# Kernel optimization log

Hardware: AMD Instinct MI355X
Metric: run time of the kernel (lower is better)

## Reference

```python
import jax, jax.numpy as jnp
import numpy as np

N_HEAD = 8
D_HEAD = 16
D_MODEL = 128
LEN_Q = 256
MEM_LEN = 256
BATCH = 4


def setup_inputs() -> dict:
    key = jax.random.key(0)
    k1, k2, k3, k4, k5 = jax.random.split(key, 5)
    h = jax.random.normal(k1, (LEN_Q, BATCH, D_MODEL), dtype=jnp.float32)
    mems = jax.random.normal(k2, (MEM_LEN, BATCH, D_MODEL), dtype=jnp.float32)
    # nn.Linear weights are [out_features, in_features]
    Wq = jax.random.normal(k3, (N_HEAD * D_HEAD, D_MODEL), dtype=jnp.float32) / np.sqrt(D_MODEL)
    Wk = jax.random.normal(k4, (N_HEAD * D_HEAD, D_MODEL), dtype=jnp.float32) / np.sqrt(D_MODEL)
    paramR = jax.random.normal(k5, (N_HEAD,), dtype=jnp.float32)
    return {"h": h, "mems": mems, "Wq": Wq, "Wk": Wk, "paramR": paramR}


def reference(h, mems, Wq, Wk, paramR):
    # h: [Lq, B, Dm], mems: [M, B, Dm]
    c = jnp.concatenate([mems, h], axis=0)  # [Lk, B, Dm]
    Lq, B = h.shape[0], h.shape[1]
    Lk = c.shape[0]
    # Linear (no bias): x @ W.T, then split heads and move to [H, B, L, Dh]
    head_q = (h @ Wq.T).reshape(Lq, B, N_HEAD, D_HEAD).transpose(2, 1, 0, 3)
    head_k = (c @ Wk.T).reshape(Lk, B, N_HEAD, D_HEAD).transpose(2, 1, 0, 3)
    # Pairwise difference: [H, B, Lq, Lk, Dh]
    diff = head_q[:, :, :, None, :] - head_k[:, :, None, :, :]
    scaled = diff * paramR[:, None, None, None, None] / jnp.pi
    # torch.sinc == jnp.sinc (normalized sinc, sinc(0)=1)
    score = jnp.abs(jnp.prod(jnp.sinc(scaled), axis=4))  # [H, B, Lq, Lk]
    # permute(2, 3, 1, 0) -> [Lq, Lk, B, H]
    return score.transpose(2, 3, 1, 0)
```

## Files before the change

### kernel.cpp

```cpp
#include <hip/hip_runtime.h>
#include <math.h>

#define LQ 256
#define MEML 256
#define LK 512
#define BB 4
#define NH 8
#define DM 128

#define IT 8
#define QSTRIDE 20

constexpr float INV2PI = 0.15915494309189535f;

__global__ __launch_bounds__(128) void proj_kernel(
    const float* __restrict__ hh, const float* __restrict__ mems,
    const float* __restrict__ Wq, const float* __restrict__ Wk,
    const float* __restrict__ paramR,
    float* __restrict__ qs, float* __restrict__ ksT)
{
    __shared__ float x[8 * 128];
    const int blk = blockIdx.x;
    const int t = threadIdx.x;
    const bool isQ = (blk < 128);
    const int row0 = isQ ? blk * 8 : (blk - 128) * 8;
    const float* __restrict__ W = isQ ? Wq : Wk;

    for (int r = 0; r < 8; ++r) {
        const int row = row0 + r;
        const float* src = isQ ? (hh + row * DM)
                               : ((row < MEML * BB) ? (mems + row * DM)
                                                    : (hh + (row - MEML * BB) * DM));
        x[r * 128 + t] = src[t];
    }
    __syncthreads();

    float acc[8] = {0, 0, 0, 0, 0, 0, 0, 0};
    const float* wrow = W + t * DM;
    for (int k = 0; k < DM; k += 4) {
        const float4 w = *(const float4*)(wrow + k);
        #pragma unroll
        for (int r = 0; r < 8; ++r) {
            acc[r] += x[r * 128 + k + 0] * w.x + x[r * 128 + k + 1] * w.y
                    + x[r * 128 + k + 2] * w.z + x[r * 128 + k + 3] * w.w;
        }
    }
    const int h = t >> 4, d = t & 15;
    const float rs = paramR[h] * INV2PI;
    if (isQ) {
        float* dst = qs + row0 * 128 + t;
        #pragma unroll
        for (int r = 0; r < 8; ++r) dst[r * 128] = acc[r] * rs;
    } else {
        #pragma unroll
        for (int r = 0; r < 8; ++r) {
            const int row = row0 + r;
            const int j = row >> 2, b = row & 3;
            ksT[((d >> 2) * LK + j) * 128 + (b * 8 + h) * 4 + (d & 3)] = acc[r] * rs;
        }
    }
}

__global__ __launch_bounds__(256, 6) void score_kernel(
    const float* __restrict__ qs, const float* __restrict__ ksT,
    float* __restrict__ out)
{
    __shared__ float qt[IT * 32 * QSTRIDE];
    const int t = threadIdx.x;
    const int bh = t & 31;
    const int js = t >> 5;
    const int key = bh >> 3;
    const int i0 = blockIdx.x * IT;
    const int j = blockIdx.y * 8 + js;

    constexpr float i2 = INV2PI * INV2PI;
    constexpr float i4 = i2 * i2;
    constexpr float i8 = i4 * i4;
    constexpr float C16 = i8 * i8;
    constexpr float EPS = 2.0e-4f * INV2PI;

    {
        const float* src = qs + i0 * 32 * 16;
        #pragma unroll
        for (int rep = 0; rep < 4; ++rep) {
            const int c4 = rep * 256 + t;
            const int row = c4 >> 2, cc = (c4 & 3) * 4;
            const float4 v = *(const float4*)(src + c4 * 4);
            *(float4*)(&qt[row * QSTRIDE + cc]) = v;
        }
    }

    float k[16];
    #pragma unroll
    for (int s = 0; s < 4; ++s) {
        const int plane = s ^ key;
        const float4 v = *(const float4*)(ksT + (plane * LK + j) * 128 + bh * 4);
        k[s * 4 + 0] = v.x; k[s * 4 + 1] = v.y;
        k[s * 4 + 2] = v.z; k[s * 4 + 3] = v.w;
    }
    __syncthreads();

    #pragma unroll
    for (int ii = 0; ii < IT; ii += 2) {
        const float* qrowA = &qt[((ii + 0) * 32 + bh) * QSTRIDE];
        const float* qrowB = &qt[((ii + 1) * 32 + bh) * QSTRIDE];
        float qa[16], qb[16];
        #pragma unroll
        for (int s = 0; s < 4; ++s) {
            const int sw = (s ^ key) << 2;
            const float4 a = *(const float4*)(qrowA + sw);
            const float4 b = *(const float4*)(qrowB + sw);
            qa[s * 4 + 0] = a.x; qa[s * 4 + 1] = a.y;
            qa[s * 4 + 2] = a.z; qa[s * 4 + 3] = a.w;
            qb[s * 4 + 0] = b.x; qb[s * 4 + 1] = b.y;
            qb[s * 4 + 2] = b.z; qb[s * 4 + 3] = b.w;
        }
        float pnA0 = 1.f, pdA0 = 1.f, pnA1 = 1.f, pdA1 = 1.f;
        float pnB0 = 1.f, pdB0 = 1.f, pnB1 = 1.f, pdB1 = 1.f;
        #pragma unroll
        for (int d = 0; d < 16; ++d) {
            const float uA = fmaxf(__builtin_fabsf(qa[d] - k[d]), EPS);
            const float uB = fmaxf(__builtin_fabsf(qb[d] - k[d]), EPS);
            const float sA = __builtin_amdgcn_sinf(uA);
            const float sB = __builtin_amdgcn_sinf(uB);
            if (d < 8) { pnA0 *= sA; pdA0 *= uA; pnB0 *= sB; pdB0 *= uB; }
            else       { pnA1 *= sA; pdA1 *= uA; pnB1 *= sB; pdB1 *= uB; }
        }
        const float rA0 = pnA0 * __builtin_amdgcn_rcpf(pdA0);
        const float rA1 = pnA1 * __builtin_amdgcn_rcpf(pdA1);
        const float rB0 = pnB0 * __builtin_amdgcn_rcpf(pdB0);
        const float rB1 = pnB1 * __builtin_amdgcn_rcpf(pdB1);
        out[((i0 + ii + 0) * LK + j) * 32 + bh] = __builtin_fabsf(rA0 * rA1) * C16;
        out[((i0 + ii + 1) * LK + j) * 32 + bh] = __builtin_fabsf(rB0 * rB1) * C16;
    }
}

extern "C" void kernel_launch(void* const* d_in, const int* in_sizes, int n_in,
                              void* d_out, int out_size, void* d_ws, size_t ws_size,
                              hipStream_t stream) {
    const float* hh     = (const float*)d_in[0];
    const float* mems   = (const float*)d_in[1];
    const float* Wq     = (const float*)d_in[2];
    const float* Wk     = (const float*)d_in[3];
    const float* paramR = (const float*)d_in[4];
    float* out = (float*)d_out;

    float* qs  = (float*)d_ws;
    float* ksT = qs + LQ * BB * DM;

    proj_kernel<<<384, 128, 0, stream>>>(hh, mems, Wq, Wk, paramR, qs, ksT);
    score_kernel<<<dim3(LQ / IT, LK / 8), 256, 0, stream>>>(qs, ksT, out);
}
```

Measured before the change: 30.73 us.

## Drop LDS staging of queries and shrink score tile to two query rows

New measurement: 37.43 us. +21.8%, slower.

```diff
diff --git a/kernel.cpp b/kernel.cpp
--- a/kernel.cpp
+++ b/kernel.cpp
@@ -7,9 +7,6 @@
 #define BB 4
 #define NH 8
 #define DM 128
-
-#define IT 8
-#define QSTRIDE 20
 
 constexpr float INV2PI = 0.15915494309189535f;
 
@@ -48,9 +45,12 @@
     const int h = t >> 4, d = t & 15;
     const float rs = paramR[h] * INV2PI;
     if (isQ) {
-        float* dst = qs + row0 * 128 + t;
         #pragma unroll
-        for (int r = 0; r < 8; ++r) dst[r * 128] = acc[r] * rs;
+        for (int r = 0; r < 8; ++r) {
+            const int row = row0 + r;
+            const int i = row >> 2, b = row & 3;
+            qs[(i * 32 + b * 8 + h) * 16 + d] = acc[r] * rs;
+        }
     } else {
         #pragma unroll
         for (int r = 0; r < 8; ++r) {
@@ -61,16 +61,14 @@
     }
 }
 
-__global__ __launch_bounds__(256, 6) void score_kernel(
+__global__ __launch_bounds__(256, 4) void score_kernel(
     const float* __restrict__ qs, const float* __restrict__ ksT,
     float* __restrict__ out)
 {
-    __shared__ float qt[IT * 32 * QSTRIDE];
     const int t = threadIdx.x;
     const int bh = t & 31;
     const int js = t >> 5;
-    const int key = bh >> 3;
-    const int i0 = blockIdx.x * IT;
+    const int i0 = blockIdx.x * 2;
     const int j = blockIdx.y * 8 + js;
 
     constexpr float i2 = INV2PI * INV2PI;
@@ -79,60 +77,45 @@
     constexpr float C16 = i8 * i8;
     constexpr float EPS = 2.0e-4f * INV2PI;
 
-    {
-        const float* src = qs + i0 * 32 * 16;
-        #pragma unroll
-        for (int rep = 0; rep < 4; ++rep) {
-            const int c4 = rep * 256 + t;
-            const int row = c4 >> 2, cc = (c4 & 3) * 4;
-            const float4 v = *(const float4*)(src + c4 * 4);
-            *(float4*)(&qt[row * QSTRIDE + cc]) = v;
-        }
-    }
-
     float k[16];
     #pragma unroll
     for (int s = 0; s < 4; ++s) {
-        const int plane = s ^ key;
-        const float4 v = *(const float4*)(ksT + (plane * LK + j) * 128 + bh * 4);
+        const float4 v = *(const float4*)(ksT + (s * LK + j) * 128 + bh * 4);
         k[s * 4 + 0] = v.x; k[s * 4 + 1] = v.y;
         k[s * 4 + 2] = v.z; k[s * 4 + 3] = v.w;
     }
-    __syncthreads();
-
-    #pragma unroll
-    for (int ii = 0; ii < IT; ii += 2) {
-        const float* qrowA = &qt[((ii + 0) * 32 + bh) * QSTRIDE];
-        const float* qrowB = &qt[((ii + 1) * 32 + bh) * QSTRIDE];
-        float qa[16], qb[16];
+    float qa[16], qb[16];
+    {
+        const float* qpa = qs + ((i0 + 0) * 32 + bh) * 16;
+        const float* qpb = qs + ((i0 + 1) * 32 + bh) * 16;
         #pragma unroll
         for (int s = 0; s < 4; ++s) {
-            const int sw = (s ^ key) << 2;
-            const float4 a = *(const float4*)(qrowA + sw);
-            const float4 b = *(const float4*)(qrowB + sw);
+            const float4 a = *(const float4*)(qpa + s * 4);
+            const float4 b = *(const float4*)(qpb + s * 4);
             qa[s * 4 + 0] = a.x; qa[s * 4 + 1] = a.y;
             qa[s * 4 + 2] = a.z; qa[s * 4 + 3] = a.w;
             qb[s * 4 + 0] = b.x; qb[s * 4 + 1] = b.y;
             qb[s * 4 + 2] = b.z; qb[s * 4 + 3] = b.w;
         }
-        float pnA0 = 1.f, pdA0 = 1.f, pnA1 = 1.f, pdA1 = 1.f;
-        float pnB0 = 1.f, pdB0 = 1.f, pnB1 = 1.f, pdB1 = 1.f;
-        #pragma unroll
-        for (int d = 0; d < 16; ++d) {
-            const float uA = fmaxf(__builtin_fabsf(qa[d] - k[d]), EPS);
-            const float uB = fmaxf(__builtin_fabsf(qb[d] - k[d]), EPS);
-            const float sA = __builtin_amdgcn_sinf(uA);
-            const float sB = __builtin_amdgcn_sinf(uB);
-            if (d < 8) { pnA0 *= sA; pdA0 *= uA; pnB0 *= sB; pdB0 *= uB; }
-            else       { pnA1 *= sA; pdA1 *= uA; pnB1 *= sB; pdB1 *= uB; }
-        }
-        const float rA0 = pnA0 * __builtin_amdgcn_rcpf(pdA0);
-        const float rA1 = pnA1 * __builtin_amdgcn_rcpf(pdA1);
-        const float rB0 = pnB0 * __builtin_amdgcn_rcpf(pdB0);
-        const float rB1 = pnB1 * __builtin_amdgcn_rcpf(pdB1);
-        out[((i0 + ii + 0) * LK + j) * 32 + bh] = __builtin_fabsf(rA0 * rA1) * C16;
-        out[((i0 + ii + 1) * LK + j) * 32 + bh] = __builtin_fabsf(rB0 * rB1) * C16;
     }
+
+    float pnA0 = 1.f, pdA0 = 1.f, pnA1 = 1.f, pdA1 = 1.f;
+    float pnB0 = 1.f, pdB0 = 1.f, pnB1 = 1.f, pdB1 = 1.f;
+    #pragma unroll
+    for (int d = 0; d < 16; ++d) {
+        const float uA = fmaxf(__builtin_fabsf(qa[d] - k[d]), EPS);
+        const float uB = fmaxf(__builtin_fabsf(qb[d] - k[d]), EPS);
+        const float sA = __builtin_amdgcn_sinf(uA);
+        const float sB = __builtin_amdgcn_sinf(uB);
+        if (d < 8) { pnA0 *= sA; pdA0 *= uA; pnB0 *= sB; pdB0 *= uB; }
+        else       { pnA1 *= sA; pdA1 *= uA; pnB1 *= sB; pdB1 *= uB; }
+    }
+    const float rA0 = pnA0 * __builtin_amdgcn_rcpf(pdA0);
+    const float rA1 = pnA1 * __builtin_amdgcn_rcpf(pdA1);
+    const float rB0 = pnB0 * __builtin_amdgcn_rcpf(pdB0);
+    const float rB1 = pnB1 * __builtin_amdgcn_rcpf(pdB1);
+    out[((i0 + 0) * LK + j) * 32 + bh] = __builtin_fabsf(rA0 * rA1) * C16;
+    out[((i0 + 1) * LK + j) * 32 + bh] = __builtin_fabsf(rB0 * rB1) * C16;
 }
 
 extern "C" void kernel_launch(void* const* d_in, const int* in_sizes, int n_in,
@@ -149,5 +132,5 @@
     float* ksT = qs + LQ * BB * DM;
 
     proj_kernel<<<384, 128, 0, stream>>>(hh, mems, Wq, Wk, paramR, qs, ksT);
-    score_kernel<<<dim3(LQ / IT, LK / 8), 256, 0, stream>>>(qs, ksT, out);
+    score_kernel<<<dim3(LQ / 2, LK / 8), 256, 0, stream>>>(qs, ksT, out);
 }
```
